# Kernel optimization log

Hardware: AMD Instinct MI355X
Metric: run time of the kernel (lower is better)

Reference implementation:

```python
import jax, jax.numpy as jnp
import numpy as np

N_ATOMS = 500_000
N_BONDS = 600_000
N_MOL = 25_000
DEG_COUNTS = [100_000, 175_000, 150_000, 75_000]  # degrees 1..4, sum = N_ATOMS
ATOM_F, BOND_F = 62, 6
HID, FP = 100, 512


def setup_inputs() -> dict:
    key = jax.random.key(0)
    ks = jax.random.split(key, 32)
    inp = {}
    inp['atom_features'] = jax.random.normal(ks[0], (N_ATOMS, ATOM_F), dtype=jnp.float32)
    inp['bond_features'] = jax.random.normal(ks[1], (N_BONDS, BOND_F), dtype=jnp.float32)
    for i, (name_a, name_b, n) in enumerate(zip(['an1','an2','an3','an4'], ['bn1','bn2','bn3','bn4'], DEG_COUNTS)):
        d = i + 1
        inp[name_a] = jax.random.randint(ks[2 + 2*i], (n, d), 0, N_ATOMS, dtype=jnp.int32)
        inp[name_b] = jax.random.randint(ks[3 + 2*i], (n, d), 0, N_BONDS, dtype=jnp.int32)
    inp['mol_ids'] = jnp.repeat(jnp.arange(N_MOL, dtype=jnp.int32), N_ATOMS // N_MOL)
    dims = [(ATOM_F, HID), (HID, HID), (HID, FP)]
    for li, (din, dout) in enumerate(dims):
        inp[f'Wself{li}'] = jax.random.normal(ks[12 + li], (din, dout), dtype=jnp.float32) * (din ** -0.5)
        inp[f'bself{li}'] = jax.random.normal(ks[15 + li], (dout,), dtype=jnp.float32) * 0.01
        inp[f'Wd{li}'] = jax.random.normal(ks[18 + li], (4, din + BOND_F, dout), dtype=jnp.float32) * ((din + BOND_F) ** -0.5)
        inp[f'bd{li}'] = jax.random.normal(ks[21 + li], (4, dout), dtype=jnp.float32) * 0.01
    return inp


def _forward(atom_features, bond_features, ans, bns, mol_ids, self_params, deg_params):
    x = atom_features
    for (Ws, bs), (Wd, bd) in zip(self_params, deg_params):
        self_logits = x @ Ws + bs                      # [N, out]
        neigh = []
        for d in range(4):                             # degrees 1..4 (structurally distinct)
            a_sum = x[ans[d]].sum(axis=1)              # [n_d, F_in]  gather + reduce over degree
            b_sum = bond_features[bns[d]].sum(axis=1)  # [n_d, BOND_F]
            h = jnp.concatenate([a_sum, b_sum], axis=1)
            neigh.append(h @ Wd[d] + bd[d])
        neighbors_logits = jnp.concatenate(neigh, axis=0)  # atoms sorted by degree
        t = neighbors_logits + self_logits
        norm = jnp.linalg.norm(t, axis=1, keepdims=True)   # F.normalize (L2, eps=1e-12)
        x = jax.nn.relu(t / jnp.maximum(norm, 1e-12))
    return jax.ops.segment_sum(x, mol_ids, num_segments=N_MOL)  # sum_and_stack


def reference(atom_features, bond_features, an1, an2, an3, an4, bn1, bn2, bn3, bn4,
              mol_ids, Wself0, bself0, Wself1, bself1, Wself2, bself2,
              Wd0, bd0, Wd1, bd1, Wd2, bd2):
    ans = (an1, an2, an3, an4)
    bns = (bn1, bn2, bn3, bn4)
    self_params = ((Wself0, bself0), (Wself1, bself1), (Wself2, bself2))
    deg_params = ((Wd0, bd0), (Wd1, bd1), (Wd2, bd2))
    return _forward(atom_features, bond_features, ans, bns, mol_ids, self_params, deg_params)
```

## Files before the change

### kernel.cpp

```cpp
#include <hip/hip_runtime.h>


#define XS 100

typedef __attribute__((ext_vector_type(8))) short short8;
typedef __attribute__((ext_vector_type(4))) float float4v;

__device__ __forceinline__ float bf2f(unsigned u) { return __uint_as_float(u << 16); }
__device__ __forceinline__ unsigned short f2bf(float f) {
    unsigned b = __float_as_uint(f);
    return (unsigned short)((b + 0x7FFFu + ((b >> 16) & 1u)) >> 16);
}
__device__ __forceinline__ unsigned pack2(float a, float b) {
    return (unsigned)f2bf(a) | ((unsigned)f2bf(b) << 16);
}
__device__ __forceinline__ void rowseg(int r, int& deg, int& seg) {
    if (r < 100000)      { deg = 1; seg = 0;      }
    else if (r < 275000) { deg = 2; seg = 100000; }
    else if (r < 425000) { deg = 3; seg = 275000; }
    else                 { deg = 4; seg = 425000; }
}

__global__ void prep_weights(const float* __restrict__ Ws, const float* __restrict__ bs,
                             const float* __restrict__ Wd, const float* __restrict__ bd,
                             int F_IN, int F_OUT, int F_OUT_PAD, int KP, int SELF_PAD,
                             unsigned short* __restrict__ Wt, float* __restrict__ bc)
{
    int id = blockIdx.x * 256 + threadIdx.x;
    int total = 4 * F_OUT_PAD * KP;
    if (id >= total) return;
    int k  = id % KP;
    int nq = (id / KP) % F_OUT_PAD;
    int dg = id / (KP * F_OUT_PAD);
    float v = 0.f;
    if (nq < F_OUT) {
        if (k < F_IN)                                   v = Ws[(size_t)k * F_OUT + nq];
        else if (k >= SELF_PAD && k < SELF_PAD + F_IN)  v = Wd[((size_t)dg * (F_IN + 6) + (k - SELF_PAD)) * F_OUT + nq];
        else if (k >= 2 * SELF_PAD && k < 2 * SELF_PAD + 6)
            v = Wd[((size_t)dg * (F_IN + 6) + F_IN + (k - 2 * SELF_PAD)) * F_OUT + nq];
    }
    Wt[id] = f2bf(v);
    if (k == 0)
        bc[dg * F_OUT_PAD + nq] = (nq < F_OUT) ? (bs[nq] + bd[(size_t)dg * F_OUT + nq]) : 0.f;
}

template<int DEG, int SP>
__device__ __forceinline__ void g256_bf16(
    unsigned short* Hs, const unsigned short* __restrict__ x,
    const float* __restrict__ bondf,
    const int* __restrict__ an, const int* __restrict__ bn,
    int seg, int B40)
{
    const int tid = threadIdx.x;
    const int ch  = tid & 31;
    const int rr  = tid >> 5;
    if (ch < 25) {
        int ai[5][DEG];
        #pragma unroll
        for (int p = 0; p < 5; ++p) {
            const int ri = B40 + rr + 8 * p;
            #pragma unroll
            for (int d = 0; d < DEG; ++d) ai[p][d] = an[(size_t)ri * DEG + d];
        }
        uint2 sv[5], nv[5][DEG];
        #pragma unroll
        for (int p = 0; p < 5; ++p) {
            const int atom = seg + B40 + rr + 8 * p;
            sv[p] = *(const uint2*)(x + (size_t)atom * XS + ch * 4);
            #pragma unroll
            for (int d = 0; d < DEG; ++d)
                nv[p][d] = *(const uint2*)(x + (size_t)ai[p][d] * XS + ch * 4);
        }
        #pragma unroll
        for (int p = 0; p < 5; ++p) {
            unsigned short* hrow = Hs + (rr + 8 * p) * SP;
            *(uint2*)(hrow + ch * 4) = sv[p];
            float s0 = 0.f, s1 = 0.f, s2 = 0.f, s3 = 0.f;
            #pragma unroll
            for (int d = 0; d < DEG; ++d) {
                s0 += bf2f(nv[p][d].x & 0xFFFFu); s1 += bf2f(nv[p][d].x >> 16);
                s2 += bf2f(nv[p][d].y & 0xFFFFu); s3 += bf2f(nv[p][d].y >> 16);
            }
            uint2 o; o.x = pack2(s0, s1); o.y = pack2(s2, s3);
            *(uint2*)(hrow + 104 + ch * 4) = o;
        }
    }
    if (tid < 40) {
        const int ri = B40 + tid;
        int bi[DEG];
        #pragma unroll
        for (int d = 0; d < DEG; ++d) bi[d] = bn[(size_t)ri * DEG + d];
        float2 v0[DEG], v1[DEG], v2[DEG];
        #pragma unroll
        for (int d = 0; d < DEG; ++d) {
            const float* bp = bondf + (size_t)bi[d] * 6;
            v0[d] = *(const float2*)bp;
            v1[d] = *(const float2*)(bp + 2);
            v2[d] = *(const float2*)(bp + 4);
        }
        float s0 = 0.f, s1 = 0.f, s2 = 0.f, s3 = 0.f, s4 = 0.f, s5 = 0.f;
        #pragma unroll
        for (int d = 0; d < DEG; ++d) {
            s0 += v0[d].x; s1 += v0[d].y; s2 += v1[d].x;
            s3 += v1[d].y; s4 += v2[d].x; s5 += v2[d].y;
        }
        unsigned short* hrow = Hs + tid * SP;
        uint4 w; w.x = pack2(s0, s1); w.y = pack2(s2, s3); w.z = pack2(s4, s5); w.w = 0;
        *(uint4*)(hrow + 208) = w;
        *(uint4*)(hrow + 216) = make_uint4(0, 0, 0, 0);
    }
    for (int i = tid; i < 80; i += 256) {
        unsigned short* p = Hs + (i >> 1) * SP + ((i & 1) ? 204 : 100);
        *(uint2*)p = make_uint2(0, 0);
    }
    for (int i = tid; i < 8 * 28; i += 256)
        *(uint4*)(Hs + (40 + i / 28) * SP + (i % 28) * 8) = make_uint4(0, 0, 0, 0);
}

template<int DEG, int SP>
__device__ __forceinline__ void g256_f32(
    unsigned short* Hs, const float* __restrict__ x,
    const float* __restrict__ bondf,
    const int* __restrict__ an, const int* __restrict__ bn,
    int seg, int B40)
{
    const int tid = threadIdx.x;
    const int ch  = tid & 31;
    const int rr  = tid >> 5;
    if (ch < 31) {
        int ai[5][DEG];
        #pragma unroll
        for (int p = 0; p < 5; ++p) {
            const int ri = B40 + rr + 8 * p;
            #pragma unroll
            for (int d = 0; d < DEG; ++d) ai[p][d] = an[(size_t)ri * DEG + d];
        }
        float2 sv[5], nv[5][DEG];
        #pragma unroll
        for (int p = 0; p < 5; ++p) {
            const int atom = seg + B40 + rr + 8 * p;
            sv[p] = *(const float2*)(x + (size_t)atom * 62 + ch * 2);
            #pragma unroll
            for (int d = 0; d < DEG; ++d)
                nv[p][d] = *(const float2*)(x + (size_t)ai[p][d] * 62 + ch * 2);
        }
        #pragma unroll
        for (int p = 0; p < 5; ++p) {
            unsigned short* hrow = Hs + (rr + 8 * p) * SP;
            *(unsigned*)(hrow + ch * 2) = pack2(sv[p].x, sv[p].y);
            float s0 = 0.f, s1 = 0.f;
            #pragma unroll
            for (int d = 0; d < DEG; ++d) { s0 += nv[p][d].x; s1 += nv[p][d].y; }
            *(unsigned*)(hrow + 64 + ch * 2) = pack2(s0, s1);
        }
    }
    if (tid < 40) {
        const int ri = B40 + tid;
        int bi[DEG];
        #pragma unroll
        for (int d = 0; d < DEG; ++d) bi[d] = bn[(size_t)ri * DEG + d];
        float2 v0[DEG], v1[DEG], v2[DEG];
        #pragma unroll
        for (int d = 0; d < DEG; ++d) {
            const float* bp = bondf + (size_t)bi[d] * 6;
            v0[d] = *(const float2*)bp;
            v1[d] = *(const float2*)(bp + 2);
            v2[d] = *(const float2*)(bp + 4);
        }
        float s0 = 0.f, s1 = 0.f, s2 = 0.f, s3 = 0.f, s4 = 0.f, s5 = 0.f;
        #pragma unroll
        for (int d = 0; d < DEG; ++d) {
            s0 += v0[d].x; s1 += v0[d].y; s2 += v1[d].x;
            s3 += v1[d].y; s4 += v2[d].x; s5 += v2[d].y;
        }
        unsigned short* hrow = Hs + tid * SP;
        uint4 w; w.x = pack2(s0, s1); w.y = pack2(s2, s3); w.z = pack2(s4, s5); w.w = 0;
        *(uint4*)(hrow + 128) = w;
        *(uint4*)(hrow + 136) = make_uint4(0, 0, 0, 0);
        *(uint4*)(hrow + 144) = make_uint4(0, 0, 0, 0);
        *(uint4*)(hrow + 152) = make_uint4(0, 0, 0, 0);
    }
    for (int i = tid; i < 80; i += 256)
        *(unsigned*)(Hs + (i >> 1) * SP + ((i & 1) ? 126 : 62)) = 0;
    for (int i = tid; i < 8 * 20; i += 256)
        *(uint4*)(Hs + (40 + i / 20) * SP + (i % 20) * 8) = make_uint4(0, 0, 0, 0);
}

template<int DEG, int SP>
__device__ __forceinline__ void g512_bf16(
    unsigned short* Hs, const unsigned short* __restrict__ x,
    const float* __restrict__ bondf,
    const int* __restrict__ an, const int* __restrict__ bn,
    int seg, int B40)
{
    const int tid = threadIdx.x;
    const int ch  = tid & 31;
    const int rg  = tid >> 5;
    if (ch < 25) {
        int ai[3][DEG];
        #pragma unroll
        for (int p = 0; p < 3; ++p) {
            const int r = rg + 16 * p;
            if (r < 40) {
                const int ri = B40 + r;
                #pragma unroll
                for (int d = 0; d < DEG; ++d) ai[p][d] = an[(size_t)ri * DEG + d];
            }
        }
        uint2 sv[3], nv[3][DEG];
        #pragma unroll
        for (int p = 0; p < 3; ++p) {
            const int r = rg + 16 * p;
            if (r < 40) {
                sv[p] = *(const uint2*)(x + (size_t)(seg + B40 + r) * XS + ch * 4);
                #pragma unroll
                for (int d = 0; d < DEG; ++d)
                    nv[p][d] = *(const uint2*)(x + (size_t)ai[p][d] * XS + ch * 4);
            }
        }
        #pragma unroll
        for (int p = 0; p < 3; ++p) {
            const int r = rg + 16 * p;
            if (r < 40) {
                unsigned short* hrow = Hs + r * SP;
                *(uint2*)(hrow + ch * 4) = sv[p];
                float s0 = 0.f, s1 = 0.f, s2 = 0.f, s3 = 0.f;
                #pragma unroll
                for (int d = 0; d < DEG; ++d) {
                    s0 += bf2f(nv[p][d].x & 0xFFFFu); s1 += bf2f(nv[p][d].x >> 16);
                    s2 += bf2f(nv[p][d].y & 0xFFFFu); s3 += bf2f(nv[p][d].y >> 16);
                }
                uint2 o; o.x = pack2(s0, s1); o.y = pack2(s2, s3);
                *(uint2*)(hrow + 104 + ch * 4) = o;
            }
        }
    } else {
        const int idx = rg * 7 + (ch - 25);
        if (idx < 40) {
            const int ri = B40 + idx;
            int bi[DEG];
            #pragma unroll
            for (int d = 0; d < DEG; ++d) bi[d] = bn[(size_t)ri * DEG + d];
            float2 v0[DEG], v1[DEG], v2[DEG];
            #pragma unroll
            for (int d = 0; d < DEG; ++d) {
                const float* bp = bondf + (size_t)bi[d] * 6;
                v0[d] = *(const float2*)bp;
                v1[d] = *(const float2*)(bp + 2);
                v2[d] = *(const float2*)(bp + 4);
            }
            float s0 = 0.f, s1 = 0.f, s2 = 0.f, s3 = 0.f, s4 = 0.f, s5 = 0.f;
            #pragma unroll
            for (int d = 0; d < DEG; ++d) {
                s0 += v0[d].x; s1 += v0[d].y; s2 += v1[d].x;
                s3 += v1[d].y; s4 += v2[d].x; s5 += v2[d].y;
            }
            unsigned short* hrow = Hs + idx * SP;
            uint4 w; w.x = pack2(s0, s1); w.y = pack2(s2, s3); w.z = pack2(s4, s5); w.w = 0;
            *(uint4*)(hrow + 208) = w;
            *(uint4*)(hrow + 216) = make_uint4(0, 0, 0, 0);
        }
    }
    for (int i = tid; i < 80; i += 512) {
        unsigned short* p = Hs + (i >> 1) * SP + ((i & 1) ? 204 : 100);
        *(uint2*)p = make_uint2(0, 0);
    }
    for (int i = tid; i < 8 * 28; i += 512)
        *(uint4*)(Hs + (40 + i / 28) * SP + (i % 28) * 8) = make_uint4(0, 0, 0, 0);
}

template<int F_IN, int F_OUT, int F_OUT_PAD, int SELF_PAD, bool LAST, bool BF16IN, int BLK>
__global__ __launch_bounds__(BLK, BLK == 512 ? 4 : 2) void layer_fused(
    const void* __restrict__ xin,
    const float* __restrict__ bondf,
    const int* __restrict__ an1, const int* __restrict__ bn1,
    const int* __restrict__ an2, const int* __restrict__ bn2,
    const int* __restrict__ an3, const int* __restrict__ bn3,
    const int* __restrict__ an4, const int* __restrict__ bn4,
    const unsigned short* __restrict__ Wt,
    const float* __restrict__ bcomb,
    unsigned short* __restrict__ xout,
    float* __restrict__ molout)
{
    constexpr int KP   = (2 * SELF_PAD + 6 + 31) & ~31;
    constexpr int SP   = KP + 8;
    constexpr int NT   = F_OUT_PAD / 16;
    constexpr int NW   = BLK / 64;
    constexpr int JMAX = (NT + NW - 1) / NW;

    __shared__ __align__(16) unsigned short Hs[48 * SP];
    __shared__ float ssqs[NW][48];
    __shared__ __align__(16) float rn48[48];

    const int R0 = blockIdx.x * 40;
    int deg, seg; rowseg(R0, deg, seg);
    const int B40 = R0 - seg;

    if constexpr (BF16IN) {
        const unsigned short* x = (const unsigned short*)xin;
        if constexpr (BLK == 256) {
            switch (deg) {
                case 1: g256_bf16<1, SP>(Hs, x, bondf, an1, bn1, seg, B40); break;
                case 2: g256_bf16<2, SP>(Hs, x, bondf, an2, bn2, seg, B40); break;
                case 3: g256_bf16<3, SP>(Hs, x, bondf, an3, bn3, seg, B40); break;
                default: g256_bf16<4, SP>(Hs, x, bondf, an4, bn4, seg, B40); break;
            }
        } else {
            switch (deg) {
                case 1: g512_bf16<1, SP>(Hs, x, bondf, an1, bn1, seg, B40); break;
                case 2: g512_bf16<2, SP>(Hs, x, bondf, an2, bn2, seg, B40); break;
                case 3: g512_bf16<3, SP>(Hs, x, bondf, an3, bn3, seg, B40); break;
                default: g512_bf16<4, SP>(Hs, x, bondf, an4, bn4, seg, B40); break;
            }
        }
    } else {
        const float* x = (const float*)xin;
        switch (deg) {
            case 1: g256_f32<1, SP>(Hs, x, bondf, an1, bn1, seg, B40); break;
            case 2: g256_f32<2, SP>(Hs, x, bondf, an2, bn2, seg, B40); break;
            case 3: g256_f32<3, SP>(Hs, x, bondf, an3, bn3, seg, B40); break;
            default: g256_f32<4, SP>(Hs, x, bondf, an4, bn4, seg, B40); break;
        }
    }
    __syncthreads();

    const int lane = threadIdx.x & 63;
    const int wv   = threadIdx.x >> 6;
    const int n16  = lane & 15;
    const int quad = lane >> 4;

    float4v acc[JMAX][3];
    #pragma unroll
    for (int j = 0; j < JMAX; ++j)
        #pragma unroll
        for (int mt = 0; mt < 3; ++mt)
            acc[j][mt] = (float4v){0.f, 0.f, 0.f, 0.f};

    const unsigned short* Wb = Wt + (size_t)(deg - 1) * F_OUT_PAD * KP;

    #pragma unroll
    for (int kk = 0; kk < KP; kk += 32) {
        short8 a[3];
        #pragma unroll
        for (int mt = 0; mt < 3; ++mt)
            a[mt] = *(const short8*)&Hs[(mt * 16 + n16) * SP + kk + quad * 8];
        short8 b[JMAX];
        #pragma unroll
        for (int j = 0; j < JMAX; ++j) {
            const int nt = wv + NW * j;
            if (nt < NT)
                b[j] = *(const short8*)(Wb + (size_t)(nt * 16 + n16) * KP + kk + quad * 8);
        }
        #pragma unroll
        for (int j = 0; j < JMAX; ++j) {
            const int nt = wv + NW * j;
            if (nt < NT)
                #pragma unroll
                for (int mt = 0; mt < 3; ++mt)
                    acc[j][mt] = __builtin_amdgcn_mfma_f32_16x16x32_bf16(
                        a[mt], b[j], acc[j][mt], 0, 0, 0);
        }
    }

    float ssq[3][4];
    #pragma unroll
    for (int mt = 0; mt < 3; ++mt)
        #pragma unroll
        for (int r = 0; r < 4; ++r) ssq[mt][r] = 0.f;

    #pragma unroll
    for (int j = 0; j < JMAX; ++j) {
        const int nt = wv + NW * j;
        if (nt < NT) {
            const float bj = bcomb[(deg - 1) * F_OUT_PAD + nt * 16 + n16];
            #pragma unroll
            for (int mt = 0; mt < 3; ++mt)
                #pragma unroll
                for (int r = 0; r < 4; ++r) {
                    float t = acc[j][mt][r] + bj;
                    acc[j][mt][r] = t;
                    ssq[mt][r] += t * t;
                }
        }
    }
    #pragma unroll
    for (int off = 1; off <= 8; off <<= 1)
        #pragma unroll
        for (int mt = 0; mt < 3; ++mt)
            #pragma unroll
            for (int r = 0; r < 4; ++r)
                ssq[mt][r] += __shfl_xor(ssq[mt][r], off);
    if (n16 == 0)
        #pragma unroll
        for (int mt = 0; mt < 3; ++mt)
            #pragma unroll
            for (int r = 0; r < 4; ++r)
                ssqs[wv][mt * 16 + quad * 4 + r] = ssq[mt][r];
    __syncthreads();

    if (threadIdx.x < 48) {
        float s = 0.f;
        #pragma unroll
        for (int w = 0; w < NW; ++w) s += ssqs[w][threadIdx.x];
        rn48[threadIdx.x] = 1.0f / fmaxf(sqrtf(s), 1e-12f);
    }
    __syncthreads();

    float rn[3][4];
    #pragma unroll
    for (int mt = 0; mt < 3; ++mt) {
        float4 v = *(const float4*)&rn48[mt * 16 + quad * 4];
        rn[mt][0] = v.x; rn[mt][1] = v.y; rn[mt][2] = v.z; rn[mt][3] = v.w;
    }

    if constexpr (!LAST) {
        #pragma unroll
        for (int j = 0; j < JMAX; ++j) {
            const int nt = wv + NW * j;
            if (nt < NT) {
                const int col = nt * 16 + n16;
                if (col < F_OUT) {
                    #pragma unroll
                    for (int mt = 0; mt < 3; ++mt)
                        #pragma unroll
                        for (int r = 0; r < 4; ++r) {
                            const int row = mt * 16 + quad * 4 + r;
                            if (row < 40) {
                                const float v = fmaxf(acc[j][mt][r] * rn[mt][r], 0.f);
                                xout[(size_t)(R0 + row) * XS + col] = f2bf(v);
                            }
                        }
                }
            }
        }
    } else {
        #pragma unroll
        for (int j = 0; j < JMAX; ++j) {
            float m0 = 0.f, m1 = 0.f;
            #pragma unroll
            for (int mt = 0; mt < 3; ++mt)
                #pragma unroll
                for (int r = 0; r < 4; ++r) {
                    const int row = mt * 16 + quad * 4 + r;
                    if (row < 40) {
                        const float v = fmaxf(acc[j][mt][r] * rn[mt][r], 0.f);
                        if (row < 20) m0 += v; else m1 += v;
                    }
                }
            m0 += __shfl_xor(m0, 16); m0 += __shfl_xor(m0, 32);
            m1 += __shfl_xor(m1, 16); m1 += __shfl_xor(m1, 32);
            if (quad == 0) {
                const int col = (wv + NW * j) * 16 + n16;
                molout[(size_t)(2 * blockIdx.x)     * 512 + col] = m0;
                molout[(size_t)(2 * blockIdx.x + 1) * 512 + col] = m1;
            }
        }
    }
}

extern "C" void kernel_launch(void* const* d_in, const int* in_sizes, int n_in,
                              void* d_out, int out_size, void* d_ws, size_t ws_size,
                              hipStream_t stream) {
    const bool sig_order = (in_sizes[3] != 100000);

    const float* atomf = (const float*)d_in[0];
    const float* bondf = (const float*)d_in[1];
    const int *an1, *bn1, *an2, *bn2, *an3, *bn3, *an4, *bn4;
    const float *Ws0, *bs0, *Wd0, *bd0;
    const float *Ws1, *bs1, *Wd1, *bd1;
    const float *Ws2, *bs2, *Wd2, *bd2;

    if (!sig_order) {
        an1 = (const int*)d_in[2];  bn1 = (const int*)d_in[3];
        an2 = (const int*)d_in[4];  bn2 = (const int*)d_in[5];
        an3 = (const int*)d_in[6];  bn3 = (const int*)d_in[7];
        an4 = (const int*)d_in[8];  bn4 = (const int*)d_in[9];
        Ws0 = (const float*)d_in[11]; bs0 = (const float*)d_in[12];
        Wd0 = (const float*)d_in[13]; bd0 = (const float*)d_in[14];
        Ws1 = (const float*)d_in[15]; bs1 = (const float*)d_in[16];
        Wd1 = (const float*)d_in[17]; bd1 = (const float*)d_in[18];
        Ws2 = (const float*)d_in[19]; bs2 = (const float*)d_in[20];
        Wd2 = (const float*)d_in[21]; bd2 = (const float*)d_in[22];
    } else {
        an1 = (const int*)d_in[2];  an2 = (const int*)d_in[3];
        an3 = (const int*)d_in[4];  an4 = (const int*)d_in[5];
        bn1 = (const int*)d_in[6];  bn2 = (const int*)d_in[7];
        bn3 = (const int*)d_in[8];  bn4 = (const int*)d_in[9];
        Ws0 = (const float*)d_in[11]; bs0 = (const float*)d_in[12];
        Ws1 = (const float*)d_in[13]; bs1 = (const float*)d_in[14];
        Ws2 = (const float*)d_in[15]; bs2 = (const float*)d_in[16];
        Wd0 = (const float*)d_in[17]; bd0 = (const float*)d_in[18];
        Wd1 = (const float*)d_in[19]; bd1 = (const float*)d_in[20];
        Wd2 = (const float*)d_in[21]; bd2 = (const float*)d_in[22];
    }

    char* w = (char*)d_ws;
    unsigned short* x1  = (unsigned short*)w;
    unsigned short* x2  = (unsigned short*)(w + 100000000);
    unsigned short* Wt0 = (unsigned short*)(w + 200000000);
    float*          bc0 = (float*)(w + 200143360);
    unsigned short* Wt1 = (unsigned short*)(w + 200145152);
    float*          bc1 = (float*)(w + 200345856);
    unsigned short* Wt2 = (unsigned short*)(w + 200347648);
    float*          bc2 = (float*)(w + 201265152);

    prep_weights<<<(4 * 112 * 160 + 255) / 256, 256, 0, stream>>>(
        Ws0, bs0, Wd0, bd0, 62, 100, 112, 160, 64, Wt0, bc0);
    prep_weights<<<(4 * 112 * 224 + 255) / 256, 256, 0, stream>>>(
        Ws1, bs1, Wd1, bd1, 100, 100, 112, 224, 104, Wt1, bc1);
    prep_weights<<<(4 * 512 * 224 + 255) / 256, 256, 0, stream>>>(
        Ws2, bs2, Wd2, bd2, 100, 512, 512, 224, 104, Wt2, bc2);

    layer_fused<62, 100, 112, 64, false, false, 256><<<12500, 256, 0, stream>>>(
        atomf, bondf, an1, bn1, an2, bn2, an3, bn3, an4, bn4,
        Wt0, bc0, x1, nullptr);
    layer_fused<100, 100, 112, 104, false, true, 256><<<12500, 256, 0, stream>>>(
        x1, bondf, an1, bn1, an2, bn2, an3, bn3, an4, bn4,
        Wt1, bc1, x2, nullptr);
    layer_fused<100, 512, 512, 104, true, true, 512><<<12500, 512, 0, stream>>>(
        x2, bondf, an1, bn1, an2, bn2, an3, bn3, an4, bn4,
        Wt2, bc2, nullptr, (float*)d_out);
}
```

Baseline: 815.8 us.

## Process two 40-row tiles per 512-thread block in hidden layers

Layers 0 and 1 are split out into a new kernel in which each 512-thread block gathers two 40-atom chunks into one 96-row shared tile. Each wave then loads a weight fragment once and reuses it across six MFMA row tiles instead of three. This halves the grid to 6251 blocks and raises weight reuse per block, but uses more shared memory and accumulator registers, and adds tail handling for degree segments with an odd chunk count. The last layer is specialised with constants so that the per-tile bounds checks on the column tiles are dropped.

```diff
diff --git a/kernel.cpp b/kernel.cpp
--- a/kernel.cpp
+++ b/kernel.cpp
@@ -49,9 +49,8 @@
     unsigned short* Hs, const unsigned short* __restrict__ x,
     const float* __restrict__ bondf,
     const int* __restrict__ an, const int* __restrict__ bn,
-    int seg, int B40)
+    int seg, int B40, int tid)
 {
-    const int tid = threadIdx.x;
     const int ch  = tid & 31;
     const int rr  = tid >> 5;
     if (ch < 25) {
@@ -122,9 +121,8 @@
     unsigned short* Hs, const float* __restrict__ x,
     const float* __restrict__ bondf,
     const int* __restrict__ an, const int* __restrict__ bn,
-    int seg, int B40)
+    int seg, int B40, int tid)
 {
-    const int tid = threadIdx.x;
     const int ch  = tid & 31;
     const int rr  = tid >> 5;
     if (ch < 31) {
@@ -269,8 +267,8 @@
         *(uint4*)(Hs + (40 + i / 28) * SP + (i % 28) * 8) = make_uint4(0, 0, 0, 0);
 }
 
-template<int F_IN, int F_OUT, int F_OUT_PAD, int SELF_PAD, bool LAST, bool BF16IN, int BLK>
-__global__ __launch_bounds__(BLK, BLK == 512 ? 4 : 2) void layer_fused(
+template<int F_IN, int SELF_PAD, bool BF16IN>
+__global__ __launch_bounds__(512, 4) void layer01(
     const void* __restrict__ xin,
     const float* __restrict__ bondf,
     const int* __restrict__ an1, const int* __restrict__ bn1,
@@ -279,47 +277,49 @@
     const int* __restrict__ an4, const int* __restrict__ bn4,
     const unsigned short* __restrict__ Wt,
     const float* __restrict__ bcomb,
-    unsigned short* __restrict__ xout,
-    float* __restrict__ molout)
+    unsigned short* __restrict__ xout)
 {
-    constexpr int KP   = (2 * SELF_PAD + 6 + 31) & ~31;
-    constexpr int SP   = KP + 8;
-    constexpr int NT   = F_OUT_PAD / 16;
-    constexpr int NW   = BLK / 64;
-    constexpr int JMAX = (NT + NW - 1) / NW;
-
-    __shared__ __align__(16) unsigned short Hs[48 * SP];
-    __shared__ float ssqs[NW][48];
-    __shared__ __align__(16) float rn48[48];
-
-    const int R0 = blockIdx.x * 40;
-    int deg, seg; rowseg(R0, deg, seg);
-    const int B40 = R0 - seg;
-
-    if constexpr (BF16IN) {
-        const unsigned short* x = (const unsigned short*)xin;
-        if constexpr (BLK == 256) {
+    constexpr int F_OUT = 100;
+    constexpr int F_OUT_PAD = 112;
+    constexpr int KP = (2 * SELF_PAD + 6 + 31) & ~31;
+    constexpr int SP = KP + 8;
+
+    __shared__ __align__(16) unsigned short Hs[96 * SP];
+    __shared__ float ssqs[7][96];
+    __shared__ __align__(16) float rn96[96];
+
+    const int b = blockIdx.x;
+    int deg, seg, pair; bool has1;
+    if (b < 1250)      { deg = 1; seg = 0;      pair = b;        has1 = true; }
+    else if (b < 3438) { deg = 2; seg = 100000; pair = b - 1250; has1 = (pair != 2187); }
+    else if (b < 5313) { deg = 3; seg = 275000; pair = b - 3438; has1 = true; }
+    else               { deg = 4; seg = 425000; pair = b - 5313; has1 = (pair != 937); }
+
+    const int half = threadIdx.x >> 8;
+    const int t    = threadIdx.x & 255;
+    const int B40  = pair * 80 + half * 40;
+    unsigned short* HsC = Hs + half * 48 * SP;
+
+    if (half == 1 && !has1) {
+        for (int i = t; i < 48 * SP / 8; i += 256)
+            ((uint4*)HsC)[i] = make_uint4(0, 0, 0, 0);
+    } else {
+        if constexpr (BF16IN) {
+            const unsigned short* x = (const unsigned short*)xin;
             switch (deg) {
-                case 1: g256_bf16<1, SP>(Hs, x, bondf, an1, bn1, seg, B40); break;
-                case 2: g256_bf16<2, SP>(Hs, x, bondf, an2, bn2, seg, B40); break;
-                case 3: g256_bf16<3, SP>(Hs, x, bondf, an3, bn3, seg, B40); break;
-                default: g256_bf16<4, SP>(Hs, x, bondf, an4, bn4, seg, B40); break;
+                case 1: g256_bf16<1, SP>(HsC, x, bondf, an1, bn1, seg, B40, t); break;
+                case 2: g256_bf16<2, SP>(HsC, x, bondf, an2, bn2, seg, B40, t); break;
+                case 3: g256_bf16<3, SP>(HsC, x, bondf, an3, bn3, seg, B40, t); break;
+                default: g256_bf16<4, SP>(HsC, x, bondf, an4, bn4, seg, B40, t); break;
             }
         } else {
+            const float* x = (const float*)xin;
             switch (deg) {
-                case 1: g512_bf16<1, SP>(Hs, x, bondf, an1, bn1, seg, B40); break;
-                case 2: g512_bf16<2, SP>(Hs, x, bondf, an2, bn2, seg, B40); break;
-                case 3: g512_bf16<3, SP>(Hs, x, bondf, an3, bn3, seg, B40); break;
-                default: g512_bf16<4, SP>(Hs, x, bondf, an4, bn4, seg, B40); break;
-            }
-        }
-    } else {
-        const float* x = (const float*)xin;
-        switch (deg) {
-            case 1: g256_f32<1, SP>(Hs, x, bondf, an1, bn1, seg, B40); break;
-            case 2: g256_f32<2, SP>(Hs, x, bondf, an2, bn2, seg, B40); break;
-            case 3: g256_f32<3, SP>(Hs, x, bondf, an3, bn3, seg, B40); break;
-            default: g256_f32<4, SP>(Hs, x, bondf, an4, bn4, seg, B40); break;
+                case 1: g256_f32<1, SP>(HsC, x, bondf, an1, bn1, seg, B40, t); break;
+                case 2: g256_f32<2, SP>(HsC, x, bondf, an2, bn2, seg, B40, t); break;
+                case 3: g256_f32<3, SP>(HsC, x, bondf, an3, bn3, seg, B40, t); break;
+                default: g256_f32<4, SP>(HsC, x, bondf, an4, bn4, seg, B40, t); break;
+            }
         }
     }
     __syncthreads();
@@ -329,6 +329,122 @@
     const int n16  = lane & 15;
     const int quad = lane >> 4;
 
+    float4v acc[6];
+    #pragma unroll
+    for (int mt = 0; mt < 6; ++mt) acc[mt] = (float4v){0.f, 0.f, 0.f, 0.f};
+
+    if (wv < 7) {
+        const unsigned short* Wr =
+            Wt + ((size_t)(deg - 1) * F_OUT_PAD + wv * 16 + n16) * KP;
+        #pragma unroll
+        for (int kk = 0; kk < KP; kk += 32) {
+            short8 bb = *(const short8*)(Wr + kk + quad * 8);
+            short8 a[6];
+            #pragma unroll
+            for (int mt = 0; mt < 6; ++mt)
+                a[mt] = *(const short8*)&Hs[(mt * 16 + n16) * SP + kk + quad * 8];
+            #pragma unroll
+            for (int mt = 0; mt < 6; ++mt)
+                acc[mt] = __builtin_amdgcn_mfma_f32_16x16x32_bf16(a[mt], bb, acc[mt], 0, 0, 0);
+        }
+    }
+
+    float ssq[6][4];
+    #pragma unroll
+    for (int mt = 0; mt < 6; ++mt)
+        #pragma unroll
+        for (int r = 0; r < 4; ++r) ssq[mt][r] = 0.f;
+
+    if (wv < 7) {
+        const float bj = bcomb[(deg - 1) * F_OUT_PAD + wv * 16 + n16];
+        #pragma unroll
+        for (int mt = 0; mt < 6; ++mt)
+            #pragma unroll
+            for (int r = 0; r < 4; ++r) {
+                float v = acc[mt][r] + bj;
+                acc[mt][r] = v;
+                ssq[mt][r] += v * v;
+            }
+        #pragma unroll
+        for (int off = 1; off <= 8; off <<= 1)
+            #pragma unroll
+            for (int mt = 0; mt < 6; ++mt)
+                #pragma unroll
+                for (int r = 0; r < 4; ++r)
+                    ssq[mt][r] += __shfl_xor(ssq[mt][r], off);
+        if (n16 == 0)
+            #pragma unroll
+            for (int mt = 0; mt < 6; ++mt)
+                #pragma unroll
+                for (int r = 0; r < 4; ++r)
+                    ssqs[wv][mt * 16 + quad * 4 + r] = ssq[mt][r];
+    }
+    __syncthreads();
+
+    if (threadIdx.x < 96) {
+        float s = 0.f;
+        #pragma unroll
+        for (int w = 0; w < 7; ++w) s += ssqs[w][threadIdx.x];
+        rn96[threadIdx.x] = 1.0f / fmaxf(sqrtf(s), 1e-12f);
+    }
+    __syncthreads();
+
+    const int col = wv * 16 + n16;
+    if (wv < 7 && col < F_OUT) {
+        #pragma unroll
+        for (int mt = 0; mt < 6; ++mt) {
+            const int chunk = mt / 3;
+            if (chunk == 0 || has1) {
+                float4 rv = *(const float4*)&rn96[mt * 16 + quad * 4];
+                const float rn_[4] = {rv.x, rv.y, rv.z, rv.w};
+                const int rowc0 = (mt % 3) * 16 + quad * 4;
+                const int gbase = seg + pair * 80 + chunk * 40 + rowc0;
+                #pragma unroll
+                for (int r = 0; r < 4; ++r) {
+                    if (rowc0 + r < 40) {
+                        const float v = fmaxf(acc[mt][r] * rn_[r], 0.f);
+                        xout[(size_t)(gbase + r) * XS + col] = f2bf(v);
+                    }
+                }
+            }
+        }
+    }
+}
+
+__global__ __launch_bounds__(512, 4) void layer_last(
+    const unsigned short* __restrict__ x,
+    const float* __restrict__ bondf,
+    const int* __restrict__ an1, const int* __restrict__ bn1,
+    const int* __restrict__ an2, const int* __restrict__ bn2,
+    const int* __restrict__ an3, const int* __restrict__ bn3,
+    const int* __restrict__ an4, const int* __restrict__ bn4,
+    const unsigned short* __restrict__ Wt,
+    const float* __restrict__ bcomb,
+    float* __restrict__ molout)
+{
+    constexpr int KP = 224, SP = 232, NW = 8, JMAX = 4;
+
+    __shared__ __align__(16) unsigned short Hs[48 * SP];
+    __shared__ float ssqs[NW][48];
+    __shared__ __align__(16) float rn48[48];
+
+    const int R0 = blockIdx.x * 40;
+    int deg, seg; rowseg(R0, deg, seg);
+    const int B40 = R0 - seg;
+
+    switch (deg) {
+        case 1: g512_bf16<1, SP>(Hs, x, bondf, an1, bn1, seg, B40); break;
+        case 2: g512_bf16<2, SP>(Hs, x, bondf, an2, bn2, seg, B40); break;
+        case 3: g512_bf16<3, SP>(Hs, x, bondf, an3, bn3, seg, B40); break;
+        default: g512_bf16<4, SP>(Hs, x, bondf, an4, bn4, seg, B40); break;
+    }
+    __syncthreads();
+
+    const int lane = threadIdx.x & 63;
+    const int wv   = threadIdx.x >> 6;
+    const int n16  = lane & 15;
+    const int quad = lane >> 4;
+
     float4v acc[JMAX][3];
     #pragma unroll
     for (int j = 0; j < JMAX; ++j)
@@ -336,7 +452,7 @@
         for (int mt = 0; mt < 3; ++mt)
             acc[j][mt] = (float4v){0.f, 0.f, 0.f, 0.f};
 
-    const unsigned short* Wb = Wt + (size_t)(deg - 1) * F_OUT_PAD * KP;
+    const unsigned short* Wb = Wt + (size_t)(deg - 1) * 512 * KP;
 
     #pragma unroll
     for (int kk = 0; kk < KP; kk += 32) {
@@ -344,22 +460,18 @@
         #pragma unroll
         for (int mt = 0; mt < 3; ++mt)
             a[mt] = *(const short8*)&Hs[(mt * 16 + n16) * SP + kk + quad * 8];
-        short8 b[JMAX];
+        short8 bfr[JMAX];
         #pragma unroll
         for (int j = 0; j < JMAX; ++j) {
             const int nt = wv + NW * j;
-            if (nt < NT)
-                b[j] = *(const short8*)(Wb + (size_t)(nt * 16 + n16) * KP + kk + quad * 8);
-        }
-        #pragma unroll
-        for (int j = 0; j < JMAX; ++j) {
-            const int nt = wv + NW * j;
-            if (nt < NT)
-                #pragma unroll
-                for (int mt = 0; mt < 3; ++mt)
-                    acc[j][mt] = __builtin_amdgcn_mfma_f32_16x16x32_bf16(
-                        a[mt], b[j], acc[j][mt], 0, 0, 0);
-        }
+            bfr[j] = *(const short8*)(Wb + (size_t)(nt * 16 + n16) * KP + kk + quad * 8);
+        }
+        #pragma unroll
+        for (int j = 0; j < JMAX; ++j)
+            #pragma unroll
+            for (int mt = 0; mt < 3; ++mt)
+                acc[j][mt] = __builtin_amdgcn_mfma_f32_16x16x32_bf16(
+                    a[mt], bfr[j], acc[j][mt], 0, 0, 0);
     }
 
     float ssq[3][4];
@@ -371,17 +483,15 @@
     #pragma unroll
     for (int j = 0; j < JMAX; ++j) {
         const int nt = wv + NW * j;
-        if (nt < NT) {
-            const float bj = bcomb[(deg - 1) * F_OUT_PAD + nt * 16 + n16];
-            #pragma unroll
-            for (int mt = 0; mt < 3; ++mt)
-                #pragma unroll
-                for (int r = 0; r < 4; ++r) {
-                    float t = acc[j][mt][r] + bj;
-                    acc[j][mt][r] = t;
-                    ssq[mt][r] += t * t;
-                }
-        }
+        const float bj = bcomb[(deg - 1) * 512 + nt * 16 + n16];
+        #pragma unroll
+        for (int mt = 0; mt < 3; ++mt)
+            #pragma unroll
+            for (int r = 0; r < 4; ++r) {
+                float v = acc[j][mt][r] + bj;
+                acc[j][mt][r] = v;
+                ssq[mt][r] += v * v;
+            }
     }
     #pragma unroll
     for (int off = 1; off <= 8; off <<= 1)
@@ -413,47 +523,25 @@
         rn[mt][0] = v.x; rn[mt][1] = v.y; rn[mt][2] = v.z; rn[mt][3] = v.w;
     }
 
-    if constexpr (!LAST) {
-        #pragma unroll
-        for (int j = 0; j < JMAX; ++j) {
-            const int nt = wv + NW * j;
-            if (nt < NT) {
-                const int col = nt * 16 + n16;
-                if (col < F_OUT) {
-                    #pragma unroll
-                    for (int mt = 0; mt < 3; ++mt)
-                        #pragma unroll
-                        for (int r = 0; r < 4; ++r) {
-                            const int row = mt * 16 + quad * 4 + r;
-                            if (row < 40) {
-                                const float v = fmaxf(acc[j][mt][r] * rn[mt][r], 0.f);
-                                xout[(size_t)(R0 + row) * XS + col] = f2bf(v);
-                            }
-                        }
+    #pragma unroll
+    for (int j = 0; j < JMAX; ++j) {
+        float m0 = 0.f, m1 = 0.f;
+        #pragma unroll
+        for (int mt = 0; mt < 3; ++mt)
+            #pragma unroll
+            for (int r = 0; r < 4; ++r) {
+                const int row = mt * 16 + quad * 4 + r;
+                if (row < 40) {
+                    const float v = fmaxf(acc[j][mt][r] * rn[mt][r], 0.f);
+                    if (row < 20) m0 += v; else m1 += v;
                 }
             }
-        }
-    } else {
-        #pragma unroll
-        for (int j = 0; j < JMAX; ++j) {
-            float m0 = 0.f, m1 = 0.f;
-            #pragma unroll
-            for (int mt = 0; mt < 3; ++mt)
-                #pragma unroll
-                for (int r = 0; r < 4; ++r) {
-                    const int row = mt * 16 + quad * 4 + r;
-                    if (row < 40) {
-                        const float v = fmaxf(acc[j][mt][r] * rn[mt][r], 0.f);
-                        if (row < 20) m0 += v; else m1 += v;
-                    }
-                }
-            m0 += __shfl_xor(m0, 16); m0 += __shfl_xor(m0, 32);
-            m1 += __shfl_xor(m1, 16); m1 += __shfl_xor(m1, 32);
-            if (quad == 0) {
-                const int col = (wv + NW * j) * 16 + n16;
-                molout[(size_t)(2 * blockIdx.x)     * 512 + col] = m0;
-                molout[(size_t)(2 * blockIdx.x + 1) * 512 + col] = m1;
-            }
+        m0 += __shfl_xor(m0, 16); m0 += __shfl_xor(m0, 32);
+        m1 += __shfl_xor(m1, 16); m1 += __shfl_xor(m1, 32);
+        if (quad == 0) {
+            const int col = (wv + NW * j) * 16 + n16;
+            molout[(size_t)(2 * blockIdx.x)     * 512 + col] = m0;
+            molout[(size_t)(2 * blockIdx.x + 1) * 512 + col] = m1;
         }
     }
 }
@@ -511,13 +599,11 @@
     prep_weights<<<(4 * 512 * 224 + 255) / 256, 256, 0, stream>>>(
         Ws2, bs2, Wd2, bd2, 100, 512, 512, 224, 104, Wt2, bc2);
 
-    layer_fused<62, 100, 112, 64, false, false, 256><<<12500, 256, 0, stream>>>(
-        atomf, bondf, an1, bn1, an2, bn2, an3, bn3, an4, bn4,
-        Wt0, bc0, x1, nullptr);
-    layer_fused<100, 100, 112, 104, false, true, 256><<<12500, 256, 0, stream>>>(
-        x1, bondf, an1, bn1, an2, bn2, an3, bn3, an4, bn4,
-        Wt1, bc1, x2, nullptr);
-    layer_fused<100, 512, 512, 104, true, true, 512><<<12500, 512, 0, stream>>>(
+    layer01<62, 64, false><<<6251, 512, 0, stream>>>(
+        atomf, bondf, an1, bn1, an2, bn2, an3, bn3, an4, bn4, Wt0, bc0, x1);
+    layer01<100, 104, true><<<6251, 512, 0, stream>>>(
+        x1, bondf, an1, bn1, an2, bn2, an3, bn3, an4, bn4, Wt1, bc1, x2);
+    layer_last<<<12500, 512, 0, stream>>>(
         x2, bondf, an1, bn1, an2, bn2, an3, bn3, an4, bn4,
-        Wt2, bc2, nullptr, (float*)d_out);
-}
+        Wt2, bc2, (float*)d_out);
+}
```

After: 778.9 us. -4.5%, faster.
